# Kernel tuning notes

Hardware: AMD Instinct MI355X
Metric: run time of the kernel (lower is better)

The kernel has to match this reference:

```python
import jax, jax.numpy as jnp
import numpy as np

B, T, NV, NH = 4, 128, 92, 4
N = NV + NH
D = 32          # d_species
H = 32          # free_nn_hidden
NUM_FORMS = 5
TOP_K = 8


def setup_inputs() -> dict:
    key = jax.random.key(0)
    ks = jax.random.split(key, 10)
    inp = {}
    inp["state"] = jax.random.uniform(ks[0], (B, T, N), dtype=jnp.float32)
    # learned parameters (per __init__)
    inp["species_emb"] = 0.1 * jax.random.normal(ks[1], (N, D), dtype=jnp.float32)
    inp["q_w"] = 0.05 * jax.random.normal(ks[2], (1 + D, D), dtype=jnp.float32)
    inp["q_b"] = jnp.zeros((D,), jnp.float32)
    inp["k_w"] = 0.05 * jax.random.normal(ks[3], (1 + D, D), dtype=jnp.float32)
    inp["k_b"] = jnp.zeros((D,), jnp.float32)
    inp["form_coefs"] = 0.05 * jax.random.normal(ks[4], (NUM_FORMS, N, N), dtype=jnp.float32)
    gates = -2.0 * jnp.ones((NUM_FORMS, N, N), jnp.float32)
    gates = gates.at[:, :NV, NV:].set(0.0)  # hidden->visible edges start open
    inp["form_gates_raw"] = gates
    inp["holling_alpha_raw"] = jnp.zeros((N,), jnp.float32)
    # free-form MLP: Linear(2+2D,H) -> GELU -> Linear(H,H) -> GELU -> Linear(H,1)
    inp["w1"] = 0.05 * jax.random.normal(ks[5], (2 + 2 * D, H), dtype=jnp.float32)
    inp["b1"] = jnp.zeros((H,), jnp.float32)
    inp["w2"] = 0.05 * jax.random.normal(ks[6], (H, H), dtype=jnp.float32)
    inp["b2"] = jnp.zeros((H,), jnp.float32)
    inp["w3"] = 0.05 * jax.random.normal(ks[7], (H, 1), dtype=jnp.float32)
    inp["b3"] = jnp.zeros((1,), jnp.float32)
    inp["r"] = jnp.zeros((N,), jnp.float32)
    return inp


def _forward(state, species_emb, q_w, q_b, k_w, k_b, form_coefs, form_gates_raw,
             holling_alpha_raw, w1, b1, w2, b2, w3, b3, r):
    Bc, Tc, Nc = state.shape
    d = species_emb.shape[1]
    gates = jax.nn.sigmoid(form_gates_raw)                  # (F,N,N)
    alpha = jax.nn.softplus(holling_alpha_raw) + 0.01       # (N,)

    xi = state[..., :, None]                                # (B,T,N,1) receiver i
    xj = state[..., None, :]                                # (B,T,1,N) sender j
    hol = xj / (1.0 + alpha * xj)                           # (B,T,1,N)
    f0 = jnp.broadcast_to(xj, (Bc, Tc, Nc, Nc))             # Linear
    f1 = xi * xj                                            # LV bilinear
    f2 = jnp.broadcast_to(hol, (Bc, Tc, Nc, Nc))            # Holling II linear
    f3 = xi * hol                                           # Holling II bilinear

    # Free NN over [x_i, x_j, s_i, s_j]: decompose first Linear to avoid the
    # (B,T,N,N,2+2D) concat; mathematically identical.
    w_xi, w_xj = w1[0], w1[1]                               # (H,), (H,)
    emb_i = species_emb @ w1[2:2 + d]                       # (N,H)
    emb_j = species_emb @ w1[2 + d:]                        # (N,H)
    h = (xi[..., None] * w_xi + xj[..., None] * w_xj
         + emb_i[None, None, :, None, :] + emb_j[None, None, None, :, :] + b1)
    h = jax.nn.gelu(h, approximate=False)
    h = jax.nn.gelu(h @ w2 + b2, approximate=False)
    f4 = (h @ w3 + b3)[..., 0]                              # (B,T,N,N)

    forms = jnp.stack([f0, f1, f2, f3, f4], axis=0)         # (F,B,T,N,N)
    w = (form_coefs * gates)[:, None, None]                 # (F,1,1,N,N)
    msgs = (w * forms).sum(axis=0)                          # (B,T,N,N)

    feats = jnp.concatenate(
        [state[..., None], jnp.broadcast_to(species_emb, (Bc, Tc, Nc, d))], axis=-1)
    q = feats @ q_w + q_b                                   # (B,T,N,D)
    k = feats @ k_w + k_b
    scores = jnp.einsum('btnd,btmd->btnm', q, k) / jnp.sqrt(jnp.float32(d))

    # top-k masked softmax over senders
    topv, _ = jax.lax.top_k(scores, TOP_K)
    thresh = topv[..., -1:]
    masked = jnp.where(scores >= thresh, scores, -jnp.inf)
    attn = jax.nn.softmax(masked, axis=-1)                  # (B,T,N,N)

    agg = (attn * msgs).sum(axis=-1)                        # (B,T,N)
    log_ratio = r + agg
    return log_ratio, attn


def reference(state, species_emb, q_w, q_b, k_w, k_b, form_coefs, form_gates_raw,
              holling_alpha_raw, w1, b1, w2, b2, w3, b3, r):
    return _forward(state, species_emb, q_w, q_b, k_w, k_b, form_coefs,
                    form_gates_raw, holling_alpha_raw, w1, b1, w2, b2, w3, b3, r)
```

## Files before the change

### kernel.cpp

```cpp
#include <hip/hip_runtime.h>
#include <math.h>

#define N_SP 96
#define D_EMB 32
#define H_MLP 32
#define NPAIR 9216
#define NBT 512
#define HROWS 48

#define WS_F_EMBI  0
#define WS_F_EMBJT 3072
#define WS_F_ALPHA 6176
#define WS_F_WG4   6272
#define WS_F_WG1   43136

typedef __attribute__((ext_vector_type(8))) short bf16x8;
typedef __attribute__((ext_vector_type(4))) float f32x4;
typedef __attribute__((ext_vector_type(4))) unsigned u32x4;

__device__ __forceinline__ float gelu_fast(float x){
  float x2 = x * x;
  float z  = x * fmaf(x2, -0.1029438824f, -2.3022077325f);
  float e  = __builtin_amdgcn_exp2f(z);
  return x * __builtin_amdgcn_rcpf(1.0f + e);
}

__device__ __forceinline__ unsigned short f2bf(float f){
  unsigned u = __builtin_bit_cast(unsigned, f);
  unsigned r = (u + 0x7FFFu + ((u >> 16) & 1u)) >> 16;
  return (unsigned short)r;
}

__device__ __forceinline__ unsigned cvt_pk_bf16(float lo, float hi){
  unsigned r;
  asm("v_cvt_pk_bf16_f32 %0, %1, %2" : "=v"(r) : "v"(lo), "v"(hi));
  return r;
}

__global__ void pre1_kernel(const float* __restrict__ emb,
                            const float* __restrict__ w1, const float* __restrict__ b1,
                            const float* __restrict__ har,
                            float* __restrict__ wsf){
  const int n = blockIdx.x;
  const int t = threadIdx.x;
  const int which = t >> 5, idx = t & 31;
  const float* e = emb + n * D_EMB;
  if (which == 0){
    float acc = b1[idx];
    #pragma unroll
    for (int u = 0; u < D_EMB; u++) acc = fmaf(e[u], w1[(2+u)*H_MLP + idx], acc);
    wsf[WS_F_EMBI + n*H_MLP + idx] = acc;
  } else {
    float acc = 0.f;
    #pragma unroll
    for (int u = 0; u < D_EMB; u++) acc = fmaf(e[u], w1[(2+D_EMB+u)*H_MLP + idx], acc);
    wsf[WS_F_EMBJT + idx*97 + n] = acc;
  }
  if (t == 0){
    float h = har[n];
    float sp = (h > 20.f) ? h : log1pf(expf(h));
    wsf[WS_F_ALPHA + n] = sp + 0.01f;
  }
}

__global__ void prewg_kernel(const float* __restrict__ fc, const float* __restrict__ fg,
                             float* __restrict__ wsf){
  int idx = blockIdx.x * 256 + threadIdx.x;
  if (idx < 5 * NPAIR){
    float g = 1.f / (1.f + expf(-fg[idx]));
    float v = fc[idx] * g;
    int f = idx / NPAIR;
    int p = idx - f * NPAIR;
    if (f < 4) wsf[WS_F_WG4 + 4*p + f] = v;
    else       wsf[WS_F_WG1 + p] = v;
  }
}

__device__ __forceinline__ void np_score2(const float* __restrict__ qiA,
                                          const float* __restrict__ qiB,
                                          const float* __restrict__ kT, int j,
                                          float* __restrict__ vA,
                                          float* __restrict__ vB){
  float accA[4], accB[4];
  #pragma unroll
  for (int l = 0; l < 4; l++){
    const float k0 = kT[(l)*97 + j];
    const float k4 = kT[(4+l)*97 + j];
    const float k8 = kT[(8+l)*97 + j];
    const float k12 = kT[(12+l)*97 + j];
    const float k16 = kT[(16+l)*97 + j];
    const float k20 = kT[(20+l)*97 + j];
    const float k24 = kT[(24+l)*97 + j];
    const float k28 = kT[(28+l)*97 + j];
    float tA = __fadd_rn(__fmul_rn(qiA[4+l], k4), __fmul_rn(qiA[l], k0));
    float tB = __fadd_rn(__fmul_rn(qiB[4+l], k4), __fmul_rn(qiB[l], k0));
    tA = __fadd_rn(__fmul_rn(qiA[8+l],  k8),  tA);
    tB = __fadd_rn(__fmul_rn(qiB[8+l],  k8),  tB);
    tA = __fadd_rn(__fmul_rn(qiA[12+l], k12), tA);
    tB = __fadd_rn(__fmul_rn(qiB[12+l], k12), tB);
    tA = __fadd_rn(__fmul_rn(qiA[16+l], k16), tA);
    tB = __fadd_rn(__fmul_rn(qiB[16+l], k16), tB);
    tA = __fadd_rn(__fmul_rn(qiA[20+l], k20), tA);
    tB = __fadd_rn(__fmul_rn(qiB[20+l], k20), tB);
    tA = __fadd_rn(__fmul_rn(qiA[24+l], k24), tA);
    tB = __fadd_rn(__fmul_rn(qiB[24+l], k24), tB);
    tA = __fadd_rn(__fmul_rn(qiA[28+l], k28), tA);
    tB = __fadd_rn(__fmul_rn(qiB[28+l], k28), tB);
    accA[l] = tA;
    accB[l] = tB;
  }
  float sA01 = __fadd_rn(accA[0], accA[1]);
  float sA23 = __fadd_rn(accA[2], accA[3]);
  float sB01 = __fadd_rn(accB[0], accB[1]);
  float sB23 = __fadd_rn(accB[2], accB[3]);
  *vA = __fdiv_rn(__fadd_rn(sA01, sA23), 5.65685424949238019521f);
  *vB = __fdiv_rn(__fadd_rn(sB01, sB23), 5.65685424949238019521f);
}

__global__ __launch_bounds__(512) void main_kernel(
    const float* __restrict__ state, const float* __restrict__ rvec,
    const float* __restrict__ emb,
    const float* __restrict__ qwg, const float* __restrict__ qbg,
    const float* __restrict__ kwg, const float* __restrict__ kbg,
    const float* __restrict__ w1, const float* __restrict__ w2g,
    const float* __restrict__ b2g, const float* __restrict__ w3g,
    const float* __restrict__ b3g,
    const float* __restrict__ wsf,
    float* __restrict__ out_lr, float* __restrict__ out_attn){

  __shared__ __align__(16) float s_embi[HROWS*H_MLP];
  __shared__ float s_embjT[H_MLP*97];
  __shared__ __align__(16) float s_q[HROWS*D_EMB];
  __shared__ float s_kT[D_EMB*97];
  __shared__ float s_x[N_SP], s_hol[N_SP];
  __shared__ float s_wxi[H_MLP], s_wxj[H_MLP], s_b2[H_MLP], s_w3[H_MLP];
  __shared__ int   s_selj[8][2][16];
  __shared__ float s_msg[8][2][16];

  const int tid  = threadIdx.x;
  const int bt   = blockIdx.x >> 1;
  const int roff = (blockIdx.x & 1) * HROWS;
  const int wave = tid >> 6, lane = tid & 63;

  for (int idx = tid; idx < HROWS*H_MLP; idx += 512)
    s_embi[idx] = wsf[WS_F_EMBI + roff*H_MLP + idx];
  for (int idx = tid; idx < H_MLP*97; idx += 512)
    s_embjT[idx] = wsf[WS_F_EMBJT + idx];
  if (tid < N_SP){
    float x = state[bt*N_SP + tid];
    s_x[tid] = x;
    float al = wsf[WS_F_ALPHA + tid];
    s_hol[tid] = x / (1.f + al * x);
  }
  if (tid >= 128 && tid < 160){
    int u = tid - 128;
    s_wxi[u] = w1[u];
    s_wxj[u] = w1[H_MLP + u];
    s_b2[u]  = b2g[u];
    s_w3[u]  = w3g[u];
  }
  __syncthreads();

  for (int t = tid; t < N_SP*D_EMB; t += 512){
    const int n = t >> 5, d2 = t & 31;
    const float* e = emb + n*D_EMB;
    float ak = __fmul_rn(s_x[n], kwg[d2]);
    #pragma unroll
    for (int u = 0; u < D_EMB; u++)
      ak = fmaf(e[u], kwg[(1+u)*D_EMB + d2], ak);
    ak = __fadd_rn(ak, kbg[d2]);
    s_kT[d2*97 + n] = ak;
  }
  for (int t = tid; t < HROWS*D_EMB; t += 512){
    const int nl = t >> 5, d2 = t & 31;
    const int n  = roff + nl;
    const float* e = emb + n*D_EMB;
    float aq = __fmul_rn(s_x[n], qwg[d2]);
    #pragma unroll
    for (int u = 0; u < D_EMB; u++)
      aq = fmaf(e[u], qwg[(1+u)*D_EMB + d2], aq);
    aq = __fadd_rn(aq, qbg[d2]);
    s_q[t] = aq;
  }

  const float b3v = b3g[0];
  const float* wg4 = wsf + WS_F_WG4;
  const float* wg1 = wsf + WS_F_WG1;

  const int l15 = lane & 15;
  const int g16 = lane >> 4;
  const int kb  = g16 * 8;
  bf16x8 w2f0, w2f1;
  #pragma unroll
  for (int e = 0; e < 8; e++){
    w2f0[e] = (short)f2bf(w2g[(kb+e)*H_MLP + l15]);
    w2f1[e] = (short)f2bf(w2g[(kb+e)*H_MLP + 16 + l15]);
  }
  __syncthreads();

  const float LOG2E = 1.44269504088896340736f;

  for (int ir = 0; ir < 3; ir++){
    const int ilA = 6*wave + 2*ir, ilB = ilA + 1;
    const int iA  = roff + ilA,    iB  = roff + ilB;

    const float* qiA = s_q + ilA*D_EMB;
    const float* qiB = s_q + ilB*D_EMB;
    float v0A, v0B, v1A = 0.f, v1B = 0.f;
    np_score2(qiA, qiB, s_kT, lane, &v0A, &v0B);
    if (lane < 32) np_score2(qiA, qiB, s_kT, 64 + lane, &v1A, &v1B);

    unsigned k0A = __builtin_bit_cast(unsigned, v0A);
    k0A = (k0A >> 31) ? ~k0A : (k0A | 0x80000000u);
    unsigned k0B = __builtin_bit_cast(unsigned, v0B);
    k0B = (k0B >> 31) ? ~k0B : (k0B | 0x80000000u);
    unsigned k1A = 0u, k1B = 0u;
    if (lane < 32){
      unsigned uA = __builtin_bit_cast(unsigned, v1A);
      k1A = (uA >> 31) ? ~uA : (uA | 0x80000000u);
      unsigned uB = __builtin_bit_cast(unsigned, v1B);
      k1B = (uB >> 31) ? ~uB : (uB | 0x80000000u);
    }

    unsigned TA = 0u, TB = 0u;
    #pragma unroll
    for (int b = 31; b >= 0; --b){
      const unsigned bit = 1u << b;
      unsigned TcA = TA | bit;
      unsigned TcB = TB | bit;
      unsigned long long a0 = __ballot(k0A >= TcA);
      unsigned long long b0 = __ballot(k0B >= TcB);
      unsigned long long a1 = __ballot(k1A >= TcA);
      unsigned long long b1 = __ballot(k1B >= TcB);
      if (__popcll(a0) + __popcll(a1) >= 8) TA = TcA;
      if (__popcll(b0) + __popcll(b1) >= 8) TB = TcB;
    }

    unsigned long long mA0 = __ballot(k0A >= TA);
    unsigned long long mA1 = __ballot(k1A >= TA);
    unsigned long long mB0 = __ballot(k0B >= TB);
    unsigned long long mB1 = __ballot(k1B >= TB);
    const int cA0 = __popcll(mA0);
    const int cB0 = __popcll(mB0);
    int r0A = -1, r1A = -1, r0B = -1, r1B = -1;
    const unsigned long long ltm = (1ull << lane) - 1ull;
    if (k0A >= TA){
      r0A = __popcll(mA0 & ltm);
      if (r0A < 16) s_selj[wave][0][r0A] = lane;
    }
    if (lane < 32 && k1A >= TA){
      r1A = cA0 + __popcll(mA1 & ltm);
      if (r1A < 16) s_selj[wave][0][r1A] = 64 + lane;
    }
    if (k0B >= TB){
      r0B = __popcll(mB0 & ltm);
      if (r0B < 16) s_selj[wave][1][r0B] = lane;
    }
    if (lane < 32 && k1B >= TB){
      r1B = cB0 + __popcll(mB1 & ltm);
      if (r1B < 16) s_selj[wave][1][r1B] = 64 + lane;
    }
    asm volatile("s_waitcnt lgkmcnt(0)" ::: "memory");

    const int cntA = cA0 + __popcll(mA1);
    const int cntB = cB0 + __popcll(mB1);
    const int ncapA = (cntA < 16) ? cntA : 16;
    const int ncapB = (cntB < 16) ? cntB : 16;
    const int jPA = s_selj[wave][0][(l15 < ncapA) ? l15 : 0];
    const int jPB = s_selj[wave][1][(l15 < ncapB) ? l15 : 0];
    const float xjA = s_x[jPA], xjB = s_x[jPB];
    const float xiA = s_x[iA],  xiB = s_x[iB];

    float4 w4vA = {0,0,0,0}, w4vB = {0,0,0,0};
    float  w1vA = 0.f, w1vB = 0.f, hjpA = 0.f, hjpB = 0.f;
    if (lane < 16){
      const int pA = iA*N_SP + jPA;
      const int pB = iB*N_SP + jPB;
      w4vA = *(const float4*)&wg4[4*pA];
      w1vA = wg1[pA];
      hjpA = s_hol[jPA];
      w4vB = *(const float4*)&wg4[4*pB];
      w1vB = wg1[pB];
      hjpB = s_hol[jPB];
    }

    u32x4 hwA, hwB;
    #pragma unroll
    for (int e2 = 0; e2 < 4; e2++){
      const int u0 = kb + 2*e2, u1 = u0 + 1;
      const float wj0 = s_wxj[u0], wj1 = s_wxj[u1];
      const float bA0 = fmaf(xiA, s_wxi[u0], s_embi[ilA*H_MLP + u0]);
      const float bA1 = fmaf(xiA, s_wxi[u1], s_embi[ilA*H_MLP + u1]);
      const float bB0 = fmaf(xiB, s_wxi[u0], s_embi[ilB*H_MLP + u0]);
      const float bB1 = fmaf(xiB, s_wxi[u1], s_embi[ilB*H_MLP + u1]);
      float pA0 = gelu_fast(fmaf(xjA, wj0, bA0 + s_embjT[u0*97 + jPA]));
      float pA1 = gelu_fast(fmaf(xjA, wj1, bA1 + s_embjT[u1*97 + jPA]));
      float pB0 = gelu_fast(fmaf(xjB, wj0, bB0 + s_embjT[u0*97 + jPB]));
      float pB1 = gelu_fast(fmaf(xjB, wj1, bB1 + s_embjT[u1*97 + jPB]));
      hwA[e2] = cvt_pk_bf16(pA0, pA1);
      hwB[e2] = cvt_pk_bf16(pB0, pB1);
    }
    const bf16x8 hfA = __builtin_bit_cast(bf16x8, hwA);
    const bf16x8 hfB = __builtin_bit_cast(bf16x8, hwB);

    f32x4 a0A = {s_b2[4*g16+0], s_b2[4*g16+1], s_b2[4*g16+2], s_b2[4*g16+3]};
    f32x4 a1A = {s_b2[16+4*g16+0], s_b2[16+4*g16+1], s_b2[16+4*g16+2], s_b2[16+4*g16+3]};
    f32x4 a0B = a0A, a1B = a1A;
    a0A = __builtin_amdgcn_mfma_f32_16x16x32_bf16(w2f0, hfA, a0A, 0, 0, 0);
    a0B = __builtin_amdgcn_mfma_f32_16x16x32_bf16(w2f0, hfB, a0B, 0, 0, 0);
    a1A = __builtin_amdgcn_mfma_f32_16x16x32_bf16(w2f1, hfA, a1A, 0, 0, 0);
    a1B = __builtin_amdgcn_mfma_f32_16x16x32_bf16(w2f1, hfB, a1B, 0, 0, 0);

    float partA = 0.f, partB = 0.f;
    #pragma unroll
    for (int r = 0; r < 4; r++){
      const float w3v = s_w3[4*g16 + r];
      partA = fmaf(gelu_fast(a0A[r]), w3v, partA);
      partB = fmaf(gelu_fast(a0B[r]), w3v, partB);
    }
    #pragma unroll
    for (int r = 0; r < 4; r++){
      const float w3v = s_w3[16 + 4*g16 + r];
      partA = fmaf(gelu_fast(a1A[r]), w3v, partA);
      partB = fmaf(gelu_fast(a1B[r]), w3v, partB);
    }
    partA += __shfl_xor(partA, 16);
    partB += __shfl_xor(partB, 16);
    partA += __shfl_xor(partA, 32);
    partB += __shfl_xor(partB, 32);

    if (lane < 16){
      const float f4A = partA + b3v;
      const float f4B = partB + b3v;
      const float msgA = w4vA.x * xjA + w4vA.y * (xiA*xjA)
                       + w4vA.z * hjpA + w4vA.w * (xiA*hjpA) + w1vA * f4A;
      const float msgB = w4vB.x * xjB + w4vB.y * (xiB*xjB)
                       + w4vB.z * hjpB + w4vB.w * (xiB*hjpB) + w1vB * f4B;
      s_msg[wave][0][lane] = msgA;
      s_msg[wave][1][lane] = msgB;
    }
    asm volatile("s_waitcnt lgkmcnt(0)" ::: "memory");

    float e0A = (k0A >= TA) ? __builtin_amdgcn_exp2f(LOG2E*v0A) : 0.f;
    float e0B = (k0B >= TB) ? __builtin_amdgcn_exp2f(LOG2E*v0B) : 0.f;
    float e1A = 0.f, e1B = 0.f;
    if (lane < 32){
      if (k1A >= TA) e1A = __builtin_amdgcn_exp2f(LOG2E*v1A);
      if (k1B >= TB) e1B = __builtin_amdgcn_exp2f(LOG2E*v1B);
    }

    float m0A = (r0A >= 0 && r0A < 16) ? s_msg[wave][0][r0A] : 0.f;
    float m1A = (r1A >= 0 && r1A < 16) ? s_msg[wave][0][r1A] : 0.f;
    float m0B = (r0B >= 0 && r0B < 16) ? s_msg[wave][1][r0B] : 0.f;
    float m1B = (r1B >= 0 && r1B < 16) ? s_msg[wave][1][r1B] : 0.f;

    float numA = e0A * m0A;
    float numB = e0B * m0B;
    if (lane < 32){ numA += e1A * m1A; numB += e1B * m1B; }
    float denA = e0A + e1A;
    float denB = e0B + e1B;
    #pragma unroll
    for (int off = 32; off; off >>= 1){
      denA += __shfl_xor(denA, off);
      denB += __shfl_xor(denB, off);
      numA += __shfl_xor(numA, off);
      numB += __shfl_xor(numB, off);
    }
    float invA = 1.0f / denA;
    float invB = 1.0f / denB;
    float* arowA = out_attn + (size_t)(bt*N_SP + iA) * N_SP;
    float* arowB = out_attn + (size_t)(bt*N_SP + iB) * N_SP;
    arowA[lane] = e0A * invA;
    arowB[lane] = e0B * invB;
    if (lane < 32){
      arowA[64 + lane] = e1A * invA;
      arowB[64 + lane] = e1B * invB;
    }
    if (lane == 0){
      out_lr[bt*N_SP + iA] = rvec[iA] + numA * invA;
      out_lr[bt*N_SP + iB] = rvec[iB] + numB * invB;
    }
  }
}

extern "C" void kernel_launch(void* const* d_in, const int* in_sizes, int n_in,
                              void* d_out, int out_size, void* d_ws, size_t ws_size,
                              hipStream_t stream){
  const float* state = (const float*)d_in[0];
  const float* emb   = (const float*)d_in[1];
  const float* qw    = (const float*)d_in[2];
  const float* qb    = (const float*)d_in[3];
  const float* kw    = (const float*)d_in[4];
  const float* kb    = (const float*)d_in[5];
  const float* fc    = (const float*)d_in[6];
  const float* fg    = (const float*)d_in[7];
  const float* har   = (const float*)d_in[8];
  const float* w1    = (const float*)d_in[9];
  const float* b1    = (const float*)d_in[10];
  const float* w2    = (const float*)d_in[11];
  const float* b2    = (const float*)d_in[12];
  const float* w3    = (const float*)d_in[13];
  const float* b3    = (const float*)d_in[14];
  const float* rv    = (const float*)d_in[15];

  float* wsf = (float*)d_ws;
  float* out_lr   = (float*)d_out;
  float* out_attn = out_lr + NBT * N_SP;

  hipLaunchKernelGGL(pre1_kernel, dim3(N_SP), dim3(64), 0, stream,
                     emb, w1, b1, har, wsf);
  hipLaunchKernelGGL(prewg_kernel, dim3(180), dim3(256), 0, stream, fc, fg, wsf);
  hipLaunchKernelGGL(main_kernel, dim3(2*NBT), dim3(512), 0, stream,
                     state, rv, emb, qw, qb, kw, kb, w1, w2, b2, w3, b3,
                     wsf, out_lr, out_attn);
}
```

Measured before the change: 102.7 us.

## Precompute Q/K in a separate kernel and split rows across smaller blocks

Adds a preqk kernel that computes Q and transposed K once per (b,t) into workspace, so the main kernel no longer recomputes the projection in every block. The main kernel now uses 256-thread blocks that each handle 16 rows (6 blocks per b,t instead of 2), which raises block count and lowers shared memory per block. Q is read directly from global memory with uniform addresses. The old path is kept as a fallback when the workspace is too small, at the cost of an extra launch and a workspace round trip.

```diff
diff --git a/kernel.cpp b/kernel.cpp
--- a/kernel.cpp
+++ b/kernel.cpp
@@ -6,6 +6,7 @@
 #define H_MLP 32
 #define NPAIR 9216
 #define NBT 512
+#define BROWS 16
 #define HROWS 48
 
 #define WS_F_EMBI  0
@@ -13,6 +14,9 @@
 #define WS_F_ALPHA 6176
 #define WS_F_WG4   6272
 #define WS_F_WG1   43136
+#define WS_F_QG    52352
+#define WS_F_KTG   1625216
+#define WS_F_END   3214464
 
 typedef __attribute__((ext_vector_type(8))) short bf16x8;
 typedef __attribute__((ext_vector_type(4))) float f32x4;
@@ -76,48 +80,344 @@
   }
 }
 
+__global__ void preqk_kernel(const float* __restrict__ state,
+                             const float* __restrict__ emb,
+                             const float* __restrict__ qwg, const float* __restrict__ qbg,
+                             const float* __restrict__ kwg, const float* __restrict__ kbg,
+                             float* __restrict__ wsf){
+  const int bt = blockIdx.x;
+  const int tid = threadIdx.x;
+  float* qg  = wsf + WS_F_QG  + bt*(N_SP*D_EMB);
+  float* ktg = wsf + WS_F_KTG + bt*3104;
+  for (int t = tid; t < N_SP*D_EMB; t += 256){
+    const int n = t >> 5, d2 = t & 31;
+    const float xn = state[bt*N_SP + n];
+    const float* e = emb + n*D_EMB;
+    float aq = __fmul_rn(xn, qwg[d2]);
+    float ak = __fmul_rn(xn, kwg[d2]);
+    #pragma unroll
+    for (int u = 0; u < D_EMB; u++){
+      aq = fmaf(e[u], qwg[(1+u)*D_EMB + d2], aq);
+      ak = fmaf(e[u], kwg[(1+u)*D_EMB + d2], ak);
+    }
+    aq = __fadd_rn(aq, qbg[d2]);
+    ak = __fadd_rn(ak, kbg[d2]);
+    qg[t] = aq;
+    ktg[d2*97 + n] = ak;
+  }
+}
+
+__device__ __forceinline__ void np_score4(const float* __restrict__ qA,
+                                          const float* __restrict__ qB,
+                                          const float* kT, int j1, int j2,
+                                          float* v0A, float* v0B,
+                                          float* v1A, float* v1B){
+  float A1[4], B1[4], A2[4], B2[4];
+  #pragma unroll
+  for (int l = 0; l < 4; l++){
+    float k1v[8], k2v[8], qa[8], qb[8];
+    #pragma unroll
+    for (int m = 0; m < 8; m++){
+      k1v[m] = kT[(4*m+l)*97 + j1];
+      k2v[m] = kT[(4*m+l)*97 + j2];
+      qa[m]  = qA[4*m+l];
+      qb[m]  = qB[4*m+l];
+    }
+    float tA1 = __fadd_rn(__fmul_rn(qa[1],k1v[1]), __fmul_rn(qa[0],k1v[0]));
+    float tB1 = __fadd_rn(__fmul_rn(qb[1],k1v[1]), __fmul_rn(qb[0],k1v[0]));
+    float tA2 = __fadd_rn(__fmul_rn(qa[1],k2v[1]), __fmul_rn(qa[0],k2v[0]));
+    float tB2 = __fadd_rn(__fmul_rn(qb[1],k2v[1]), __fmul_rn(qb[0],k2v[0]));
+    #pragma unroll
+    for (int m = 2; m < 8; m++){
+      tA1 = __fadd_rn(__fmul_rn(qa[m],k1v[m]), tA1);
+      tB1 = __fadd_rn(__fmul_rn(qb[m],k1v[m]), tB1);
+      tA2 = __fadd_rn(__fmul_rn(qa[m],k2v[m]), tA2);
+      tB2 = __fadd_rn(__fmul_rn(qb[m],k2v[m]), tB2);
+    }
+    A1[l]=tA1; B1[l]=tB1; A2[l]=tA2; B2[l]=tB2;
+  }
+  const float S = 5.65685424949238019521f;
+  *v0A = __fdiv_rn(__fadd_rn(__fadd_rn(A1[0],A1[1]), __fadd_rn(A1[2],A1[3])), S);
+  *v0B = __fdiv_rn(__fadd_rn(__fadd_rn(B1[0],B1[1]), __fadd_rn(B1[2],B1[3])), S);
+  *v1A = __fdiv_rn(__fadd_rn(__fadd_rn(A2[0],A2[1]), __fadd_rn(A2[2],A2[3])), S);
+  *v1B = __fdiv_rn(__fadd_rn(__fadd_rn(B2[0],B2[1]), __fadd_rn(B2[2],B2[3])), S);
+}
+
+__global__ __launch_bounds__(256) void main_kernel(
+    const float* __restrict__ state, const float* __restrict__ rvec,
+    const float* __restrict__ w2g, const float* __restrict__ b3g,
+    const float* __restrict__ w1, const float* __restrict__ b2g,
+    const float* __restrict__ w3g,
+    const float* __restrict__ wsf,
+    float* __restrict__ out_lr, float* __restrict__ out_attn){
+
+  __shared__ float s_kT[3104];
+  __shared__ float s_embjT[3104];
+  __shared__ __align__(16) float s_embi[BROWS*H_MLP];
+  __shared__ float s_x[N_SP], s_hol[N_SP];
+  __shared__ float s_wxi[H_MLP], s_wxj[H_MLP], s_b2[H_MLP], s_w3[H_MLP];
+  __shared__ int   s_selj[4][2][16];
+  __shared__ float s_msg[4][2][16];
+
+  const int tid  = threadIdx.x;
+  const int bt   = blockIdx.x / 6;
+  const int roff = (blockIdx.x - 6*bt) * BROWS;
+  const int wave = tid >> 6, lane = tid & 63;
+
+  const float* ktg = wsf + WS_F_KTG + bt*3104;
+  for (int t = tid; t < 3104; t += 256){
+    s_kT[t]    = ktg[t];
+    s_embjT[t] = wsf[WS_F_EMBJT + t];
+  }
+  for (int t = tid; t < BROWS*H_MLP; t += 256)
+    s_embi[t] = wsf[WS_F_EMBI + roff*H_MLP + t];
+  if (tid < N_SP){
+    float x = state[bt*N_SP + tid];
+    s_x[tid] = x;
+    float al = wsf[WS_F_ALPHA + tid];
+    s_hol[tid] = x / (1.f + al * x);
+  }
+  if (tid >= 96 && tid < 128){
+    int u = tid - 96;
+    s_wxi[u] = w1[u];
+    s_wxj[u] = w1[H_MLP + u];
+    s_b2[u]  = b2g[u];
+    s_w3[u]  = w3g[u];
+  }
+
+  const float b3v = b3g[0];
+  const float* wg4 = wsf + WS_F_WG4;
+  const float* wg1 = wsf + WS_F_WG1;
+  const float* qg  = wsf + WS_F_QG + bt*(N_SP*D_EMB);
+
+  const int l15 = lane & 15;
+  const int g16 = lane >> 4;
+  const int kb  = g16 * 8;
+  bf16x8 w2f0, w2f1;
+  #pragma unroll
+  for (int e = 0; e < 8; e++){
+    w2f0[e] = (short)f2bf(w2g[(kb+e)*H_MLP + l15]);
+    w2f1[e] = (short)f2bf(w2g[(kb+e)*H_MLP + 16 + l15]);
+  }
+  __syncthreads();
+
+  const float LOG2E = 1.44269504088896340736f;
+  const int j2 = (lane < 32) ? (64 + lane) : 95;
+
+  for (int ir = 0; ir < 2; ir++){
+    const int ilA = 4*wave + 2*ir, ilB = ilA + 1;
+    const int iA  = roff + ilA,    iB  = roff + ilB;
+    const int iAu = __builtin_amdgcn_readfirstlane(iA);
+    const int iBu = __builtin_amdgcn_readfirstlane(iB);
+    const float* qA = qg + iAu*D_EMB;
+    const float* qB = qg + iBu*D_EMB;
+
+    float v0A, v0B, v1A, v1B;
+    np_score4(qA, qB, s_kT, lane, j2, &v0A, &v0B, &v1A, &v1B);
+
+    unsigned k0A = __builtin_bit_cast(unsigned, v0A);
+    k0A = (k0A >> 31) ? ~k0A : (k0A | 0x80000000u);
+    unsigned k0B = __builtin_bit_cast(unsigned, v0B);
+    k0B = (k0B >> 31) ? ~k0B : (k0B | 0x80000000u);
+    unsigned k1A = 0u, k1B = 0u;
+    if (lane < 32){
+      unsigned uA = __builtin_bit_cast(unsigned, v1A);
+      k1A = (uA >> 31) ? ~uA : (uA | 0x80000000u);
+      unsigned uB = __builtin_bit_cast(unsigned, v1B);
+      k1B = (uB >> 31) ? ~uB : (uB | 0x80000000u);
+    }
+
+    unsigned TA = 0u, TB = 0u;
+    #pragma unroll
+    for (int b = 31; b >= 0; --b){
+      const unsigned bit = 1u << b;
+      unsigned TcA = TA | bit;
+      unsigned TcB = TB | bit;
+      unsigned long long a0 = __ballot(k0A >= TcA);
+      unsigned long long b0 = __ballot(k0B >= TcB);
+      unsigned long long a1 = __ballot(k1A >= TcA);
+      unsigned long long b1 = __ballot(k1B >= TcB);
+      if (__popcll(a0) + __popcll(a1) >= 8) TA = TcA;
+      if (__popcll(b0) + __popcll(b1) >= 8) TB = TcB;
+    }
+
+    unsigned long long mA0 = __ballot(k0A >= TA);
+    unsigned long long mA1 = __ballot(k1A >= TA);
+    unsigned long long mB0 = __ballot(k0B >= TB);
+    unsigned long long mB1 = __ballot(k1B >= TB);
+    const int cA0 = __popcll(mA0);
+    const int cB0 = __popcll(mB0);
+    int r0A = -1, r1A = -1, r0B = -1, r1B = -1;
+    const unsigned long long ltm = (1ull << lane) - 1ull;
+    if (k0A >= TA){
+      r0A = __popcll(mA0 & ltm);
+      if (r0A < 16) s_selj[wave][0][r0A] = lane;
+    }
+    if (lane < 32 && k1A >= TA){
+      r1A = cA0 + __popcll(mA1 & ltm);
+      if (r1A < 16) s_selj[wave][0][r1A] = 64 + lane;
+    }
+    if (k0B >= TB){
+      r0B = __popcll(mB0 & ltm);
+      if (r0B < 16) s_selj[wave][1][r0B] = lane;
+    }
+    if (lane < 32 && k1B >= TB){
+      r1B = cB0 + __popcll(mB1 & ltm);
+      if (r1B < 16) s_selj[wave][1][r1B] = 64 + lane;
+    }
+    asm volatile("s_waitcnt lgkmcnt(0)" ::: "memory");
+
+    const int cntA = cA0 + __popcll(mA1);
+    const int cntB = cB0 + __popcll(mB1);
+    const int ncapA = (cntA < 16) ? cntA : 16;
+    const int ncapB = (cntB < 16) ? cntB : 16;
+    const int jPA = s_selj[wave][0][(l15 < ncapA) ? l15 : 0];
+    const int jPB = s_selj[wave][1][(l15 < ncapB) ? l15 : 0];
+    const float xjA = s_x[jPA], xjB = s_x[jPB];
+    const float xiA = s_x[iA],  xiB = s_x[iB];
+
+    float4 w4vA = {0,0,0,0}, w4vB = {0,0,0,0};
+    float  w1vA = 0.f, w1vB = 0.f, hjpA = 0.f, hjpB = 0.f;
+    if (lane < 16){
+      const int pA = iA*N_SP + jPA;
+      const int pB = iB*N_SP + jPB;
+      w4vA = *(const float4*)&wg4[4*pA];
+      w1vA = wg1[pA];
+      hjpA = s_hol[jPA];
+      w4vB = *(const float4*)&wg4[4*pB];
+      w1vB = wg1[pB];
+      hjpB = s_hol[jPB];
+    }
+
+    u32x4 hwA, hwB;
+    #pragma unroll
+    for (int e2 = 0; e2 < 4; e2++){
+      const int u0 = kb + 2*e2, u1 = u0 + 1;
+      const float wj0 = s_wxj[u0], wj1 = s_wxj[u1];
+      const float bA0 = fmaf(xiA, s_wxi[u0], s_embi[ilA*H_MLP + u0]);
+      const float bA1 = fmaf(xiA, s_wxi[u1], s_embi[ilA*H_MLP + u1]);
+      const float bB0 = fmaf(xiB, s_wxi[u0], s_embi[ilB*H_MLP + u0]);
+      const float bB1 = fmaf(xiB, s_wxi[u1], s_embi[ilB*H_MLP + u1]);
+      float pA0 = gelu_fast(fmaf(xjA, wj0, bA0 + s_embjT[u0*97 + jPA]));
+      float pA1 = gelu_fast(fmaf(xjA, wj1, bA1 + s_embjT[u1*97 + jPA]));
+      float pB0 = gelu_fast(fmaf(xjB, wj0, bB0 + s_embjT[u0*97 + jPB]));
+      float pB1 = gelu_fast(fmaf(xjB, wj1, bB1 + s_embjT[u1*97 + jPB]));
+      hwA[e2] = cvt_pk_bf16(pA0, pA1);
+      hwB[e2] = cvt_pk_bf16(pB0, pB1);
+    }
+    const bf16x8 hfA = __builtin_bit_cast(bf16x8, hwA);
+    const bf16x8 hfB = __builtin_bit_cast(bf16x8, hwB);
+
+    f32x4 a0A = {s_b2[4*g16+0], s_b2[4*g16+1], s_b2[4*g16+2], s_b2[4*g16+3]};
+    f32x4 a1A = {s_b2[16+4*g16+0], s_b2[16+4*g16+1], s_b2[16+4*g16+2], s_b2[16+4*g16+3]};
+    f32x4 a0B = a0A, a1B = a1A;
+    a0A = __builtin_amdgcn_mfma_f32_16x16x32_bf16(w2f0, hfA, a0A, 0, 0, 0);
+    a0B = __builtin_amdgcn_mfma_f32_16x16x32_bf16(w2f0, hfB, a0B, 0, 0, 0);
+    a1A = __builtin_amdgcn_mfma_f32_16x16x32_bf16(w2f1, hfA, a1A, 0, 0, 0);
+    a1B = __builtin_amdgcn_mfma_f32_16x16x32_bf16(w2f1, hfB, a1B, 0, 0, 0);
+
+    float partA = 0.f, partB = 0.f;
+    #pragma unroll
+    for (int r = 0; r < 4; r++){
+      const float w3v = s_w3[4*g16 + r];
+      partA = fmaf(gelu_fast(a0A[r]), w3v, partA);
+      partB = fmaf(gelu_fast(a0B[r]), w3v, partB);
+    }
+    #pragma unroll
+    for (int r = 0; r < 4; r++){
+      const float w3v = s_w3[16 + 4*g16 + r];
+      partA = fmaf(gelu_fast(a1A[r]), w3v, partA);
+      partB = fmaf(gelu_fast(a1B[r]), w3v, partB);
+    }
+    partA += __shfl_xor(partA, 16);
+    partB += __shfl_xor(partB, 16);
+    partA += __shfl_xor(partA, 32);
+    partB += __shfl_xor(partB, 32);
+
+    if (lane < 16){
+      const float f4A = partA + b3v;
+      const float f4B = partB + b3v;
+      const float msgA = w4vA.x * xjA + w4vA.y * (xiA*xjA)
+                       + w4vA.z * hjpA + w4vA.w * (xiA*hjpA) + w1vA * f4A;
+      const float msgB = w4vB.x * xjB + w4vB.y * (xiB*xjB)
+                       + w4vB.z * hjpB + w4vB.w * (xiB*hjpB) + w1vB * f4B;
+      s_msg[wave][0][lane] = msgA;
+      s_msg[wave][1][lane] = msgB;
+    }
+    asm volatile("s_waitcnt lgkmcnt(0)" ::: "memory");
+
+    float e0A = (k0A >= TA) ? __builtin_amdgcn_exp2f(LOG2E*v0A) : 0.f;
+    float e0B = (k0B >= TB) ? __builtin_amdgcn_exp2f(LOG2E*v0B) : 0.f;
+    float e1A = 0.f, e1B = 0.f;
+    if (lane < 32){
+      if (k1A >= TA) e1A = __builtin_amdgcn_exp2f(LOG2E*v1A);
+      if (k1B >= TB) e1B = __builtin_amdgcn_exp2f(LOG2E*v1B);
+    }
+
+    float m0A = (r0A >= 0 && r0A < 16) ? s_msg[wave][0][r0A] : 0.f;
+    float m1A = (r1A >= 0 && r1A < 16) ? s_msg[wave][0][r1A] : 0.f;
+    float m0B = (r0B >= 0 && r0B < 16) ? s_msg[wave][1][r0B] : 0.f;
+    float m1B = (r1B >= 0 && r1B < 16) ? s_msg[wave][1][r1B] : 0.f;
+
+    float numA = e0A * m0A;
+    float numB = e0B * m0B;
+    if (lane < 32){ numA += e1A * m1A; numB += e1B * m1B; }
+    float denA = e0A + e1A;
+    float denB = e0B + e1B;
+    #pragma unroll
+    for (int off = 32; off; off >>= 1){
+      denA += __shfl_xor(denA, off);
+      denB += __shfl_xor(denB, off);
+      numA += __shfl_xor(numA, off);
+      numB += __shfl_xor(numB, off);
+    }
+    float invA = 1.0f / denA;
+    float invB = 1.0f / denB;
+    float* arowA = out_attn + (size_t)(bt*N_SP + iA) * N_SP;
+    float* arowB = out_attn + (size_t)(bt*N_SP + iB) * N_SP;
+    arowA[lane] = e0A * invA;
+    arowB[lane] = e0B * invB;
+    if (lane < 32){
+      arowA[64 + lane] = e1A * invA;
+      arowB[64 + lane] = e1B * invB;
+    }
+    if (lane == 0){
+      out_lr[bt*N_SP + iA] = rvec[iA] + numA * invA;
+      out_lr[bt*N_SP + iB] = rvec[iB] + numB * invB;
+    }
+  }
+}
+
 __device__ __forceinline__ void np_score2(const float* __restrict__ qiA,
                                           const float* __restrict__ qiB,
-                                          const float* __restrict__ kT, int j,
+                                          const float* kT, int j,
                                           float* __restrict__ vA,
                                           float* __restrict__ vB){
   float accA[4], accB[4];
   #pragma unroll
   for (int l = 0; l < 4; l++){
-    const float k0 = kT[(l)*97 + j];
-    const float k4 = kT[(4+l)*97 + j];
-    const float k8 = kT[(8+l)*97 + j];
-    const float k12 = kT[(12+l)*97 + j];
-    const float k16 = kT[(16+l)*97 + j];
-    const float k20 = kT[(20+l)*97 + j];
-    const float k24 = kT[(24+l)*97 + j];
-    const float k28 = kT[(28+l)*97 + j];
-    float tA = __fadd_rn(__fmul_rn(qiA[4+l], k4), __fmul_rn(qiA[l], k0));
-    float tB = __fadd_rn(__fmul_rn(qiB[4+l], k4), __fmul_rn(qiB[l], k0));
-    tA = __fadd_rn(__fmul_rn(qiA[8+l],  k8),  tA);
-    tB = __fadd_rn(__fmul_rn(qiB[8+l],  k8),  tB);
-    tA = __fadd_rn(__fmul_rn(qiA[12+l], k12), tA);
-    tB = __fadd_rn(__fmul_rn(qiB[12+l], k12), tB);
-    tA = __fadd_rn(__fmul_rn(qiA[16+l], k16), tA);
-    tB = __fadd_rn(__fmul_rn(qiB[16+l], k16), tB);
-    tA = __fadd_rn(__fmul_rn(qiA[20+l], k20), tA);
-    tB = __fadd_rn(__fmul_rn(qiB[20+l], k20), tB);
-    tA = __fadd_rn(__fmul_rn(qiA[24+l], k24), tA);
-    tB = __fadd_rn(__fmul_rn(qiB[24+l], k24), tB);
-    tA = __fadd_rn(__fmul_rn(qiA[28+l], k28), tA);
-    tB = __fadd_rn(__fmul_rn(qiB[28+l], k28), tB);
-    accA[l] = tA;
-    accB[l] = tB;
-  }
-  float sA01 = __fadd_rn(accA[0], accA[1]);
-  float sA23 = __fadd_rn(accA[2], accA[3]);
-  float sB01 = __fadd_rn(accB[0], accB[1]);
-  float sB23 = __fadd_rn(accB[2], accB[3]);
-  *vA = __fdiv_rn(__fadd_rn(sA01, sA23), 5.65685424949238019521f);
-  *vB = __fdiv_rn(__fadd_rn(sB01, sB23), 5.65685424949238019521f);
-}
-
-__global__ __launch_bounds__(512) void main_kernel(
+    float kv[8], qa[8], qb[8];
+    #pragma unroll
+    for (int m = 0; m < 8; m++){
+      kv[m] = kT[(4*m+l)*97 + j];
+      qa[m] = qiA[4*m+l];
+      qb[m] = qiB[4*m+l];
+    }
+    float tA = __fadd_rn(__fmul_rn(qa[1],kv[1]), __fmul_rn(qa[0],kv[0]));
+    float tB = __fadd_rn(__fmul_rn(qb[1],kv[1]), __fmul_rn(qb[0],kv[0]));
+    #pragma unroll
+    for (int m = 2; m < 8; m++){
+      tA = __fadd_rn(__fmul_rn(qa[m],kv[m]), tA);
+      tB = __fadd_rn(__fmul_rn(qb[m],kv[m]), tB);
+    }
+    accA[l] = tA; accB[l] = tB;
+  }
+  const float S = 5.65685424949238019521f;
+  *vA = __fdiv_rn(__fadd_rn(__fadd_rn(accA[0],accA[1]), __fadd_rn(accA[2],accA[3])), S);
+  *vB = __fdiv_rn(__fadd_rn(__fadd_rn(accB[0],accB[1]), __fadd_rn(accB[2],accB[3])), S);
+}
+
+__global__ __launch_bounds__(512) void main_kernel_fb(
     const float* __restrict__ state, const float* __restrict__ rvec,
     const float* __restrict__ emb,
     const float* __restrict__ qwg, const float* __restrict__ qbg,
@@ -129,9 +429,9 @@
     float* __restrict__ out_lr, float* __restrict__ out_attn){
 
   __shared__ __align__(16) float s_embi[HROWS*H_MLP];
-  __shared__ float s_embjT[H_MLP*97];
+  __shared__ float s_embjT[3104];
   __shared__ __align__(16) float s_q[HROWS*D_EMB];
-  __shared__ float s_kT[D_EMB*97];
+  __shared__ float s_kT[3104];
   __shared__ float s_x[N_SP], s_hol[N_SP];
   __shared__ float s_wxi[H_MLP], s_wxj[H_MLP], s_b2[H_MLP], s_w3[H_MLP];
   __shared__ int   s_selj[8][2][16];
@@ -144,7 +444,7 @@
 
   for (int idx = tid; idx < HROWS*H_MLP; idx += 512)
     s_embi[idx] = wsf[WS_F_EMBI + roff*H_MLP + idx];
-  for (int idx = tid; idx < H_MLP*97; idx += 512)
+  for (int idx = tid; idx < 3104; idx += 512)
     s_embjT[idx] = wsf[WS_F_EMBJT + idx];
   if (tid < N_SP){
     float x = state[bt*N_SP + tid];
@@ -410,7 +710,15 @@
   hipLaunchKernelGGL(pre1_kernel, dim3(N_SP), dim3(64), 0, stream,
                      emb, w1, b1, har, wsf);
   hipLaunchKernelGGL(prewg_kernel, dim3(180), dim3(256), 0, stream, fc, fg, wsf);
-  hipLaunchKernelGGL(main_kernel, dim3(2*NBT), dim3(512), 0, stream,
-                     state, rv, emb, qw, qb, kw, kb, w1, w2, b2, w3, b3,
-                     wsf, out_lr, out_attn);
-}
+
+  if (ws_size >= (size_t)WS_F_END * sizeof(float)){
+    hipLaunchKernelGGL(preqk_kernel, dim3(NBT), dim3(256), 0, stream,
+                       state, emb, qw, qb, kw, kb, wsf);
+    hipLaunchKernelGGL(main_kernel, dim3(6*NBT), dim3(256), 0, stream,
+                       state, rv, w2, b3, w1, b2, w3, wsf, out_lr, out_attn);
+  } else {
+    hipLaunchKernelGGL(main_kernel_fb, dim3(2*NBT), dim3(512), 0, stream,
+                       state, rv, emb, qw, qb, kw, kb, w1, w2, b2, w3, b3,
+                       wsf, out_lr, out_attn);
+  }
+}
```

New measurement: 102.7 us. About the same (+0.0%).

## Precompute Q/K per timestep in prepass and split main kernel into smaller blocks

Applied to the files above, without the earlier changes.

Merges the three preprocessing kernels into one launch and adds a per-(b,t) Q and transposed-K projection stage that writes to workspace. Before, each of two main blocks per timestep recomputed K for all species. The main kernel now uses 256-thread blocks covering 16 receiver rows each, giving six blocks per timestep. It reads precomputed K into shared memory and Q directly from global memory, and stores the sender embedding table as bf16 in shared memory. This removes redundant projection work and improves occupancy, at the cost of extra global workspace traffic and reduced precision in the MLP input term.

```diff
diff --git a/kernel.cpp b/kernel.cpp
--- a/kernel.cpp
+++ b/kernel.cpp
@@ -6,13 +6,16 @@
 #define H_MLP 32
 #define NPAIR 9216
 #define NBT 512
-#define HROWS 48
+#define BROWS 16
 
 #define WS_F_EMBI  0
 #define WS_F_EMBJT 3072
 #define WS_F_ALPHA 6176
 #define WS_F_WG4   6272
 #define WS_F_WG1   43136
+#define WS_F_QG    52352
+#define WS_F_KTG   1625216
+#define WS_F_END   3214464
 
 typedef __attribute__((ext_vector_type(8))) short bf16x8;
 typedef __attribute__((ext_vector_type(4))) float f32x4;
@@ -30,6 +33,10 @@
   unsigned r = (u + 0x7FFFu + ((u >> 16) & 1u)) >> 16;
   return (unsigned short)r;
 }
+__device__ __forceinline__ float bf2f(unsigned short s){
+  unsigned u = ((unsigned)s) << 16;
+  return __builtin_bit_cast(float, u);
+}
 
 __device__ __forceinline__ unsigned cvt_pk_bf16(float lo, float hi){
   unsigned r;
@@ -37,155 +44,164 @@
   return r;
 }
 
-__global__ void pre1_kernel(const float* __restrict__ emb,
-                            const float* __restrict__ w1, const float* __restrict__ b1,
-                            const float* __restrict__ har,
-                            float* __restrict__ wsf){
-  const int n = blockIdx.x;
-  const int t = threadIdx.x;
-  const int which = t >> 5, idx = t & 31;
-  const float* e = emb + n * D_EMB;
-  if (which == 0){
-    float acc = b1[idx];
-    #pragma unroll
-    for (int u = 0; u < D_EMB; u++) acc = fmaf(e[u], w1[(2+u)*H_MLP + idx], acc);
-    wsf[WS_F_EMBI + n*H_MLP + idx] = acc;
-  } else {
-    float acc = 0.f;
-    #pragma unroll
-    for (int u = 0; u < D_EMB; u++) acc = fmaf(e[u], w1[(2+D_EMB+u)*H_MLP + idx], acc);
-    wsf[WS_F_EMBJT + idx*97 + n] = acc;
-  }
-  if (t == 0){
-    float h = har[n];
-    float sp = (h > 20.f) ? h : log1pf(expf(h));
-    wsf[WS_F_ALPHA + n] = sp + 0.01f;
-  }
-}
-
-__global__ void prewg_kernel(const float* __restrict__ fc, const float* __restrict__ fg,
-                             float* __restrict__ wsf){
-  int idx = blockIdx.x * 256 + threadIdx.x;
-  if (idx < 5 * NPAIR){
-    float g = 1.f / (1.f + expf(-fg[idx]));
-    float v = fc[idx] * g;
-    int f = idx / NPAIR;
-    int p = idx - f * NPAIR;
-    if (f < 4) wsf[WS_F_WG4 + 4*p + f] = v;
-    else       wsf[WS_F_WG1 + p] = v;
-  }
-}
-
-__device__ __forceinline__ void np_score2(const float* __restrict__ qiA,
-                                          const float* __restrict__ qiB,
-                                          const float* __restrict__ kT, int j,
-                                          float* __restrict__ vA,
-                                          float* __restrict__ vB){
-  float accA[4], accB[4];
-  #pragma unroll
-  for (int l = 0; l < 4; l++){
-    const float k0 = kT[(l)*97 + j];
-    const float k4 = kT[(4+l)*97 + j];
-    const float k8 = kT[(8+l)*97 + j];
-    const float k12 = kT[(12+l)*97 + j];
-    const float k16 = kT[(16+l)*97 + j];
-    const float k20 = kT[(20+l)*97 + j];
-    const float k24 = kT[(24+l)*97 + j];
-    const float k28 = kT[(28+l)*97 + j];
-    float tA = __fadd_rn(__fmul_rn(qiA[4+l], k4), __fmul_rn(qiA[l], k0));
-    float tB = __fadd_rn(__fmul_rn(qiB[4+l], k4), __fmul_rn(qiB[l], k0));
-    tA = __fadd_rn(__fmul_rn(qiA[8+l],  k8),  tA);
-    tB = __fadd_rn(__fmul_rn(qiB[8+l],  k8),  tB);
-    tA = __fadd_rn(__fmul_rn(qiA[12+l], k12), tA);
-    tB = __fadd_rn(__fmul_rn(qiB[12+l], k12), tB);
-    tA = __fadd_rn(__fmul_rn(qiA[16+l], k16), tA);
-    tB = __fadd_rn(__fmul_rn(qiB[16+l], k16), tB);
-    tA = __fadd_rn(__fmul_rn(qiA[20+l], k20), tA);
-    tB = __fadd_rn(__fmul_rn(qiB[20+l], k20), tB);
-    tA = __fadd_rn(__fmul_rn(qiA[24+l], k24), tA);
-    tB = __fadd_rn(__fmul_rn(qiB[24+l], k24), tB);
-    tA = __fadd_rn(__fmul_rn(qiA[28+l], k28), tA);
-    tB = __fadd_rn(__fmul_rn(qiB[28+l], k28), tB);
-    accA[l] = tA;
-    accB[l] = tB;
-  }
-  float sA01 = __fadd_rn(accA[0], accA[1]);
-  float sA23 = __fadd_rn(accA[2], accA[3]);
-  float sB01 = __fadd_rn(accB[0], accB[1]);
-  float sB23 = __fadd_rn(accB[2], accB[3]);
-  *vA = __fdiv_rn(__fadd_rn(sA01, sA23), 5.65685424949238019521f);
-  *vB = __fdiv_rn(__fadd_rn(sB01, sB23), 5.65685424949238019521f);
-}
-
-__global__ __launch_bounds__(512) void main_kernel(
-    const float* __restrict__ state, const float* __restrict__ rvec,
+__global__ __launch_bounds__(256) void pre_all_kernel(
+    const float* __restrict__ state,
     const float* __restrict__ emb,
     const float* __restrict__ qwg, const float* __restrict__ qbg,
     const float* __restrict__ kwg, const float* __restrict__ kbg,
-    const float* __restrict__ w1, const float* __restrict__ w2g,
-    const float* __restrict__ b2g, const float* __restrict__ w3g,
-    const float* __restrict__ b3g,
+    const float* __restrict__ w1, const float* __restrict__ b1,
+    const float* __restrict__ har,
+    const float* __restrict__ fc, const float* __restrict__ fg,
+    float* __restrict__ wsf){
+  __shared__ float s_e[N_SP*D_EMB];
+  __shared__ float s_qw[1056], s_kw[1056];
+  __shared__ float s_qb[32], s_kb[32];
+
+  const int blk = blockIdx.x;
+  const int tid = threadIdx.x;
+
+  if (blk < NBT){
+    const int bt = blk;
+    float* qg  = wsf + WS_F_QG  + bt*(N_SP*D_EMB);
+    float* ktg = wsf + WS_F_KTG + bt*3104;
+    for (int t = tid; t < N_SP*D_EMB; t += 256) s_e[t] = emb[t];
+    for (int t = tid; t < 1056; t += 256){ s_qw[t] = qwg[t]; s_kw[t] = kwg[t]; }
+    if (tid < 32){ s_qb[tid] = qbg[tid]; s_kb[tid] = kbg[tid]; }
+    __syncthreads();
+
+    const int wave = tid >> 6, lane = tid & 63;
+    const int d2   = lane & 31;
+    const bool isq = (lane < 32);
+    const float* w = isq ? s_qw : s_kw;
+    const float  bias = isq ? s_qb[d2] : s_kb[d2];
+    for (int rr = 0; rr < 24; rr++){
+      const int n = 24*wave + rr;
+      const float xn = state[bt*N_SP + n];
+      float acc = __fmul_rn(xn, w[d2]);
+      #pragma unroll
+      for (int u = 0; u < D_EMB; u++)
+        acc = fmaf(s_e[n*D_EMB + u], w[(1+u)*D_EMB + d2], acc);
+      acc = __fadd_rn(acc, bias);
+      if (isq) qg[n*D_EMB + d2] = acc;
+      else     ktg[d2*97 + n]   = acc;
+    }
+  } else if (blk < NBT + 24){
+    const int gidx = (blk - NBT)*256 + tid;
+    const int n = gidx >> 6;
+    const int t = gidx & 63;
+    const int which = t >> 5, idx = t & 31;
+    const float* e = emb + n * D_EMB;
+    if (which == 0){
+      float acc = b1[idx];
+      #pragma unroll
+      for (int u = 0; u < D_EMB; u++) acc = fmaf(e[u], w1[(2+u)*H_MLP + idx], acc);
+      wsf[WS_F_EMBI + n*H_MLP + idx] = acc;
+    } else {
+      float acc = 0.f;
+      #pragma unroll
+      for (int u = 0; u < D_EMB; u++) acc = fmaf(e[u], w1[(2+D_EMB+u)*H_MLP + idx], acc);
+      wsf[WS_F_EMBJT + idx*97 + n] = acc;
+    }
+    if (t == 0){
+      float h = har[n];
+      float sp = (h > 20.f) ? h : log1pf(expf(h));
+      wsf[WS_F_ALPHA + n] = sp + 0.01f;
+    }
+  } else {
+    int idx = (blk - NBT - 24) * 256 + tid;
+    if (idx < 5 * NPAIR){
+      float g = 1.f / (1.f + expf(-fg[idx]));
+      float v = fc[idx] * g;
+      int f = idx / NPAIR;
+      int p = idx - f * NPAIR;
+      if (f < 4) wsf[WS_F_WG4 + 4*p + f] = v;
+      else       wsf[WS_F_WG1 + p] = v;
+    }
+  }
+}
+
+__device__ __forceinline__ void np_score4(const float* __restrict__ qA,
+                                          const float* __restrict__ qB,
+                                          const float* kT, int j1, int j2,
+                                          float* v0A, float* v0B,
+                                          float* v1A, float* v1B){
+  float A1[4], B1[4], A2[4], B2[4];
+  #pragma unroll
+  for (int l = 0; l < 4; l++){
+    float k1v[8], k2v[8], qa[8], qb[8];
+    #pragma unroll
+    for (int m = 0; m < 8; m++){
+      k1v[m] = kT[(4*m+l)*97 + j1];
+      k2v[m] = kT[(4*m+l)*97 + j2];
+      qa[m]  = qA[4*m+l];
+      qb[m]  = qB[4*m+l];
+    }
+    float tA1 = __fadd_rn(__fmul_rn(qa[1],k1v[1]), __fmul_rn(qa[0],k1v[0]));
+    float tB1 = __fadd_rn(__fmul_rn(qb[1],k1v[1]), __fmul_rn(qb[0],k1v[0]));
+    float tA2 = __fadd_rn(__fmul_rn(qa[1],k2v[1]), __fmul_rn(qa[0],k2v[0]));
+    float tB2 = __fadd_rn(__fmul_rn(qb[1],k2v[1]), __fmul_rn(qb[0],k2v[0]));
+    #pragma unroll
+    for (int m = 2; m < 8; m++){
+      tA1 = __fadd_rn(__fmul_rn(qa[m],k1v[m]), tA1);
+      tB1 = __fadd_rn(__fmul_rn(qb[m],k1v[m]), tB1);
+      tA2 = __fadd_rn(__fmul_rn(qa[m],k2v[m]), tA2);
+      tB2 = __fadd_rn(__fmul_rn(qb[m],k2v[m]), tB2);
+    }
+    A1[l]=tA1; B1[l]=tB1; A2[l]=tA2; B2[l]=tB2;
+  }
+  const float S = 5.65685424949238019521f;
+  *v0A = __fdiv_rn(__fadd_rn(__fadd_rn(A1[0],A1[1]), __fadd_rn(A1[2],A1[3])), S);
+  *v0B = __fdiv_rn(__fadd_rn(__fadd_rn(B1[0],B1[1]), __fadd_rn(B1[2],B1[3])), S);
+  *v1A = __fdiv_rn(__fadd_rn(__fadd_rn(A2[0],A2[1]), __fadd_rn(A2[2],A2[3])), S);
+  *v1B = __fdiv_rn(__fadd_rn(__fadd_rn(B2[0],B2[1]), __fadd_rn(B2[2],B2[3])), S);
+}
+
+__global__ __launch_bounds__(256) void main_kernel(
+    const float* __restrict__ state, const float* __restrict__ rvec,
+    const float* __restrict__ w2g, const float* __restrict__ b3g,
+    const float* __restrict__ w1, const float* __restrict__ b2g,
+    const float* __restrict__ w3g,
     const float* __restrict__ wsf,
     float* __restrict__ out_lr, float* __restrict__ out_attn){
 
-  __shared__ __align__(16) float s_embi[HROWS*H_MLP];
-  __shared__ float s_embjT[H_MLP*97];
-  __shared__ __align__(16) float s_q[HROWS*D_EMB];
-  __shared__ float s_kT[D_EMB*97];
+  __shared__ float s_kT[3104];
+  __shared__ unsigned short s_embjT16[3104];
+  __shared__ __align__(16) float s_embi[BROWS*H_MLP];
   __shared__ float s_x[N_SP], s_hol[N_SP];
   __shared__ float s_wxi[H_MLP], s_wxj[H_MLP], s_b2[H_MLP], s_w3[H_MLP];
-  __shared__ int   s_selj[8][2][16];
-  __shared__ float s_msg[8][2][16];
+  __shared__ int   s_selj[4][2][16];
+  __shared__ float s_msg[4][2][16];
 
   const int tid  = threadIdx.x;
-  const int bt   = blockIdx.x >> 1;
-  const int roff = (blockIdx.x & 1) * HROWS;
+  const int bt   = blockIdx.x / 6;
+  const int roff = (blockIdx.x - 6*bt) * BROWS;
   const int wave = tid >> 6, lane = tid & 63;
 
-  for (int idx = tid; idx < HROWS*H_MLP; idx += 512)
-    s_embi[idx] = wsf[WS_F_EMBI + roff*H_MLP + idx];
-  for (int idx = tid; idx < H_MLP*97; idx += 512)
-    s_embjT[idx] = wsf[WS_F_EMBJT + idx];
+  const float* ktg = wsf + WS_F_KTG + bt*3104;
+  for (int t = tid; t < 3104; t += 256){
+    s_kT[t]       = ktg[t];
+    s_embjT16[t]  = f2bf(wsf[WS_F_EMBJT + t]);
+  }
+  for (int t = tid; t < BROWS*H_MLP; t += 256)
+    s_embi[t] = wsf[WS_F_EMBI + roff*H_MLP + t];
   if (tid < N_SP){
     float x = state[bt*N_SP + tid];
     s_x[tid] = x;
     float al = wsf[WS_F_ALPHA + tid];
     s_hol[tid] = x / (1.f + al * x);
   }
-  if (tid >= 128 && tid < 160){
-    int u = tid - 128;
+  if (tid >= 96 && tid < 128){
+    int u = tid - 96;
     s_wxi[u] = w1[u];
     s_wxj[u] = w1[H_MLP + u];
     s_b2[u]  = b2g[u];
     s_w3[u]  = w3g[u];
   }
-  __syncthreads();
-
-  for (int t = tid; t < N_SP*D_EMB; t += 512){
-    const int n = t >> 5, d2 = t & 31;
-    const float* e = emb + n*D_EMB;
-    float ak = __fmul_rn(s_x[n], kwg[d2]);
-    #pragma unroll
-    for (int u = 0; u < D_EMB; u++)
-      ak = fmaf(e[u], kwg[(1+u)*D_EMB + d2], ak);
-    ak = __fadd_rn(ak, kbg[d2]);
-    s_kT[d2*97 + n] = ak;
-  }
-  for (int t = tid; t < HROWS*D_EMB; t += 512){
-    const int nl = t >> 5, d2 = t & 31;
-    const int n  = roff + nl;
-    const float* e = emb + n*D_EMB;
-    float aq = __fmul_rn(s_x[n], qwg[d2]);
-    #pragma unroll
-    for (int u = 0; u < D_EMB; u++)
-      aq = fmaf(e[u], qwg[(1+u)*D_EMB + d2], aq);
-    aq = __fadd_rn(aq, qbg[d2]);
-    s_q[t] = aq;
-  }
 
   const float b3v = b3g[0];
   const float* wg4 = wsf + WS_F_WG4;
   const float* wg1 = wsf + WS_F_WG1;
+  const float* qg  = wsf + WS_F_QG + bt*(N_SP*D_EMB);
 
   const int l15 = lane & 15;
   const int g16 = lane >> 4;
@@ -199,16 +215,18 @@
   __syncthreads();
 
   const float LOG2E = 1.44269504088896340736f;
-
-  for (int ir = 0; ir < 3; ir++){
-    const int ilA = 6*wave + 2*ir, ilB = ilA + 1;
+  const int j2 = (lane < 32) ? (64 + lane) : 95;
+
+  for (int ir = 0; ir < 2; ir++){
+    const int ilA = 4*wave + 2*ir, ilB = ilA + 1;
     const int iA  = roff + ilA,    iB  = roff + ilB;
-
-    const float* qiA = s_q + ilA*D_EMB;
-    const float* qiB = s_q + ilB*D_EMB;
-    float v0A, v0B, v1A = 0.f, v1B = 0.f;
-    np_score2(qiA, qiB, s_kT, lane, &v0A, &v0B);
-    if (lane < 32) np_score2(qiA, qiB, s_kT, 64 + lane, &v1A, &v1B);
+    const int iAu = __builtin_amdgcn_readfirstlane(iA);
+    const int iBu = __builtin_amdgcn_readfirstlane(iB);
+    const float* qA = qg + iAu*D_EMB;
+    const float* qB = qg + iBu*D_EMB;
+
+    float v0A, v0B, v1A, v1B;
+    np_score4(qA, qB, s_kT, lane, j2, &v0A, &v0B, &v1A, &v1B);
 
     unsigned k0A = __builtin_bit_cast(unsigned, v0A);
     k0A = (k0A >> 31) ? ~k0A : (k0A | 0x80000000u);
@@ -293,10 +311,10 @@
       const float bA1 = fmaf(xiA, s_wxi[u1], s_embi[ilA*H_MLP + u1]);
       const float bB0 = fmaf(xiB, s_wxi[u0], s_embi[ilB*H_MLP + u0]);
       const float bB1 = fmaf(xiB, s_wxi[u1], s_embi[ilB*H_MLP + u1]);
-      float pA0 = gelu_fast(fmaf(xjA, wj0, bA0 + s_embjT[u0*97 + jPA]));
-      float pA1 = gelu_fast(fmaf(xjA, wj1, bA1 + s_embjT[u1*97 + jPA]));
-      float pB0 = gelu_fast(fmaf(xjB, wj0, bB0 + s_embjT[u0*97 + jPB]));
-      float pB1 = gelu_fast(fmaf(xjB, wj1, bB1 + s_embjT[u1*97 + jPB]));
+      float pA0 = gelu_fast(fmaf(xjA, wj0, bA0 + bf2f(s_embjT16[u0*97 + jPA])));
+      float pA1 = gelu_fast(fmaf(xjA, wj1, bA1 + bf2f(s_embjT16[u1*97 + jPA])));
+      float pB0 = gelu_fast(fmaf(xjB, wj0, bB0 + bf2f(s_embjT16[u0*97 + jPB])));
+      float pB1 = gelu_fast(fmaf(xjB, wj1, bB1 + bf2f(s_embjT16[u1*97 + jPB])));
       hwA[e2] = cvt_pk_bf16(pA0, pA1);
       hwB[e2] = cvt_pk_bf16(pB0, pB1);
     }
@@ -407,10 +425,8 @@
   float* out_lr   = (float*)d_out;
   float* out_attn = out_lr + NBT * N_SP;
 
-  hipLaunchKernelGGL(pre1_kernel, dim3(N_SP), dim3(64), 0, stream,
-                     emb, w1, b1, har, wsf);
-  hipLaunchKernelGGL(prewg_kernel, dim3(180), dim3(256), 0, stream, fc, fg, wsf);
-  hipLaunchKernelGGL(main_kernel, dim3(2*NBT), dim3(512), 0, stream,
-                     state, rv, emb, qw, qb, kw, kb, w1, w2, b2, w3, b3,
-                     wsf, out_lr, out_attn);
-}
+  hipLaunchKernelGGL(pre_all_kernel, dim3(NBT + 24 + 180), dim3(256), 0, stream,
+                     state, emb, qw, qb, kw, kb, w1, b1, har, fc, fg, wsf);
+  hipLaunchKernelGGL(main_kernel, dim3(6*NBT), dim3(256), 0, stream,
+                     state, rv, w2, b3, w1, b2, w3, wsf, out_lr, out_attn);
+}
```

Measured after the change: 97.28 us. 1.06x faster.
